# Kernel optimization log

Measured on AMD Instinct MI355X. Metric: run time of the kernel, lower is better.

## Reference

```python
import jax, jax.numpy as jnp
from jax import lax
import numpy as np

N = 87296
NUM_CLASSES = 91
IOU_THRESH = 0.6
MAX_OUT = 100
IMG = 2048.0


def setup_inputs() -> dict:
    key = jax.random.key(0)
    k1, k2, k3, k4, k5 = jax.random.split(key, 5)
    class_logits = jax.random.normal(k1, (N, NUM_CLASSES), dtype=jnp.float32)
    box_regression = jax.random.normal(k2, (N, 4), dtype=jnp.float32)
    box_ctrness = jax.random.normal(k3, (N, 1), dtype=jnp.float32)
    # anchors: valid x1,y1,x2,y2 boxes inside a 2048x2048 image
    ctr = jax.random.uniform(k4, (N, 2), dtype=jnp.float32) * IMG
    wh = jax.random.uniform(k5, (N, 2), dtype=jnp.float32) * 64.0 + 8.0
    anchors = jnp.concatenate([ctr - 0.5 * wh, ctr + 0.5 * wh], axis=1)
    return {"class_logits": class_logits, "box_regression": box_regression,
            "box_ctrness": box_ctrness, "anchors": anchors}


def _decode(rel_codes, anchors):
    # torchvision BoxLinearCoder(normalize_by_size=True).decode
    ctr_x = 0.5 * (anchors[:, 0] + anchors[:, 2])
    ctr_y = 0.5 * (anchors[:, 1] + anchors[:, 3])
    w = anchors[:, 2] - anchors[:, 0]
    h = anchors[:, 3] - anchors[:, 1]
    dl = rel_codes[:, 0] * w
    dt = rel_codes[:, 1] * h
    dr = rel_codes[:, 2] * w
    db = rel_codes[:, 3] * h
    return jnp.stack([ctr_x - dl, ctr_y - dt, ctr_x + dr, ctr_y + db], axis=1)


def _nms_keep(boxes, scores, iou_thresh, max_out):
    # torchvision.ops.nms truncated to max_out; returns indices sorted by score.
    areas = jnp.maximum(boxes[:, 2] - boxes[:, 0], 0.0) * jnp.maximum(boxes[:, 3] - boxes[:, 1], 0.0)

    def body(i, state):
        cur_scores, keep = state
        idx = jnp.argmax(cur_scores)
        keep = keep.at[i].set(idx.astype(jnp.int32))
        b = boxes[idx]
        ix1 = jnp.maximum(b[0], boxes[:, 0])
        iy1 = jnp.maximum(b[1], boxes[:, 1])
        ix2 = jnp.minimum(b[2], boxes[:, 2])
        iy2 = jnp.minimum(b[3], boxes[:, 3])
        inter = jnp.maximum(ix2 - ix1, 0.0) * jnp.maximum(iy2 - iy1, 0.0)
        iou = inter / (areas[idx] + areas - inter)
        # suppress boxes with IoU > thresh (includes the selected box itself)
        cur_scores = jnp.where(iou > iou_thresh, -jnp.inf, cur_scores)
        return cur_scores, keep

    keep0 = jnp.zeros((max_out,), jnp.int32)
    _, keep = lax.fori_loop(0, max_out, body, (scores, keep0))
    return keep


def reference(class_logits, box_regression, box_ctrness, anchors):
    pred_boxes = _decode(box_regression, anchors)              # [N,4]
    cls_scores = jax.nn.sigmoid(class_logits)                  # [N,C]
    ctr_scores = jax.nn.sigmoid(box_ctrness[:, 0])             # [N]
    scores = jnp.sqrt(cls_scores * ctr_scores[:, None])        # [N,C]
    max_scores = jnp.max(scores, axis=1)                       # [N]
    labels = jnp.argmax(scores, axis=1)                        # [N]
    keep = _nms_keep(pred_boxes, max_scores, IOU_THRESH, MAX_OUT)
    return pred_boxes[keep], labels[keep], max_scores[keep]
```

## Files before the change

### kernel.cpp

```cpp
#include <hip/hip_runtime.h>
#include <math.h>

#define N_ANCH 87296
#define NCLS 91
#define NBINS 4096
#define K_CAND 256
#define CAP 512
#define MAX_OUT 100
#define IOU_TH 0.6f
#define T2 1024


__device__ __forceinline__ float sigmoidf_(float x) {
    return 1.0f / (1.0f + expf(-x));
}

__global__ void score_kernel(const float* __restrict__ logits,
                             const float* __restrict__ ctr,
                             float* __restrict__ scores) {
    __shared__ float lds[2 * 64 * 91];
    const int tid  = threadIdx.x;
    const int lane = tid & 63;
    const int w    = tid >> 6;
    const int rowbase = blockIdx.x * 128 + w * 64;

    const float4* g4 = (const float4*)logits + (size_t)rowbase * 91 / 4;
    float4* l4 = (float4*)(lds + w * 5824);
    #pragma unroll
    for (int k = 0; k < 23; ++k) {
        int idx = k * 64 + lane;
        if (idx < 1456) l4[idx] = g4[idx];
    }
    __syncthreads();

    const int i = rowbase + lane;
    const float* row = lds + w * 5824 + lane * 91;
    float m = row[0];
    #pragma unroll
    for (int j = 1; j < NCLS; ++j) m = fmaxf(m, row[j]);
    scores[i] = sqrtf(sigmoidf_(m) * sigmoidf_(ctr[i]));
}

__global__ void __launch_bounds__(T2)
select_nms_kernel(const float* __restrict__ scores,
                  const float* __restrict__ logits,
                  const float* __restrict__ boxreg,
                  const float* __restrict__ anchors,
                  float* __restrict__ out) {
    __shared__ unsigned hist[NBINS];
    __shared__ float    cs[CAP];
    __shared__ int      cidx[CAP];
    __shared__ unsigned cnt;
    __shared__ int      fbin;
    __shared__ float    s_best[16];
    __shared__ int      s_bid[16];
    __shared__ float    s_box[5];
    __shared__ int      s_lab;

    const int tid  = threadIdx.x;
    const int lane = tid & 63;
    const int wid  = tid >> 6;

    for (int b = tid; b < NBINS; b += T2) hist[b] = 0u;
    if (tid == 0) cnt = 0u;
    __syncthreads();

    const float4* s4 = (const float4*)scores;
    #pragma unroll
    for (int k = 0; k < 22; ++k) {
        int idx = k * T2 + tid;
        if (idx < N_ANCH / 4) {
            float4 v = s4[idx];
            int b0 = min(max((int)(v.x * (float)NBINS), 0), NBINS - 1);
            int b1 = min(max((int)(v.y * (float)NBINS), 0), NBINS - 1);
            int b2 = min(max((int)(v.z * (float)NBINS), 0), NBINS - 1);
            int b3 = min(max((int)(v.w * (float)NBINS), 0), NBINS - 1);
            atomicAdd(&hist[b0], 1u);
            atomicAdd(&hist[b1], 1u);
            atomicAdd(&hist[b2], 1u);
            atomicAdd(&hist[b3], 1u);
        }
    }
    __syncthreads();

    if (tid < 64) {
        const uint4* h4 = (const uint4*)hist;
        uint4 c[16];
        #pragma unroll
        for (int q = 0; q < 16; ++q) c[q] = h4[lane * 16 + q];

        unsigned local = 0;
        #pragma unroll
        for (int q = 0; q < 16; ++q) local += c[q].x + c[q].y + c[q].z + c[q].w;

        unsigned p = local;
        #pragma unroll
        for (int d = 1; d < 64; d <<= 1) {
            unsigned t = (unsigned)__shfl_down((int)p, d, 64);
            if (lane + d < 64) p += t;
        }
        unsigned long long mask = __ballot(p >= K_CAND);
        int L = 63 - __clzll(mask);
        unsigned sufAbove = (unsigned)__shfl((int)p, L + 1, 64);
        if (L == 63) sufAbove = 0u;

        if (lane == L) {
            unsigned cum = sufAbove;
            int fb = L * 64;
            bool found = false;
            #pragma unroll
            for (int q = 15; q >= 0; --q) {
                cum += c[q].w; if (!found && cum >= K_CAND) { fb = L * 64 + q * 4 + 3; found = true; }
                cum += c[q].z; if (!found && cum >= K_CAND) { fb = L * 64 + q * 4 + 2; found = true; }
                cum += c[q].y; if (!found && cum >= K_CAND) { fb = L * 64 + q * 4 + 1; found = true; }
                cum += c[q].x; if (!found && cum >= K_CAND) { fb = L * 64 + q * 4 + 0; found = true; }
            }
            fbin = fb;
        }
    }
    __syncthreads();
    const int FB = fbin;

    #pragma unroll
    for (int k = 0; k < 22; ++k) {
        int idx = k * T2 + tid;
        if (idx < N_ANCH / 4) {
            float4 v = s4[idx];
            float vv[4] = {v.x, v.y, v.z, v.w};
            #pragma unroll
            for (int c = 0; c < 4; ++c) {
                float s = vv[c];
                int b = min(max((int)(s * (float)NBINS), 0), NBINS - 1);
                if (b >= FB) {
                    unsigned pos = atomicAdd(&cnt, 1u);
                    if (pos < CAP) { cs[pos] = s; cidx[pos] = idx * 4 + c; }
                }
            }
        }
    }
    __syncthreads();
    const int M = (int)min(cnt, (unsigned)CAP);

    float SC, X1, Y1, X2, Y2, AR;
    int LAB;
    if (tid < M) {
        int i = cidx[tid];
        SC = cs[tid];
        const float* row = logits + (long)i * NCLS;
        float m = row[0];
        int lab = 0;
        #pragma unroll
        for (int j = 1; j < NCLS; ++j) {
            float v = row[j];
            if (v > m) { m = v; lab = j; }
        }
        LAB = lab;
        float a0 = anchors[i * 4 + 0], a1 = anchors[i * 4 + 1];
        float a2 = anchors[i * 4 + 2], a3 = anchors[i * 4 + 3];
        float cx = 0.5f * (a0 + a2);
        float cy = 0.5f * (a1 + a3);
        float w  = a2 - a0;
        float h  = a3 - a1;
        float r0 = boxreg[i * 4 + 0], r1 = boxreg[i * 4 + 1];
        float r2 = boxreg[i * 4 + 2], r3 = boxreg[i * 4 + 3];
        X1 = cx - r0 * w;
        Y1 = cy - r1 * h;
        X2 = cx + r2 * w;
        Y2 = cy + r3 * h;
        AR = fmaxf(X2 - X1, 0.0f) * fmaxf(Y2 - Y1, 0.0f);
    } else {
        SC = -INFINITY;
        X1 = Y1 = X2 = Y2 = AR = 0.0f;
        LAB = 0;
    }
    __syncthreads();

    for (int it = 0; it < MAX_OUT; ++it) {
        float b = SC;
        int id = tid;
        #pragma unroll
        for (int d = 32; d >= 1; d >>= 1) {
            float ob = __shfl_xor(b, d, 64);
            int   oid = __shfl_xor(id, d, 64);
            if (ob > b) { b = ob; id = oid; }
        }
        if (lane == 0) { s_best[wid] = b; s_bid[wid] = id; }
        __syncthreads();
        float gb = s_best[0];
        int gid = s_bid[0];
        #pragma unroll
        for (int w = 1; w < 16; ++w) {
            if (s_best[w] > gb) { gb = s_best[w]; gid = s_bid[w]; }
        }
        if (tid == gid) {
            s_box[0] = X1; s_box[1] = Y1; s_box[2] = X2; s_box[3] = Y2;
            s_box[4] = AR; s_lab = LAB;
        }
        __syncthreads();
        float sx1 = s_box[0], sy1 = s_box[1], sx2 = s_box[2], sy2 = s_box[3];
        float sar = s_box[4];
        int   slab = s_lab;

        if (tid == 0) {
            out[it * 4 + 0] = sx1;
            out[it * 4 + 1] = sy1;
            out[it * 4 + 2] = sx2;
            out[it * 4 + 3] = sy2;
            out[4 * MAX_OUT + it] = (float)slab;
            out[5 * MAX_OUT + it] = gb;
        }

        if (sar == 0.0f) {
            for (int r = it + 1 + tid; r < MAX_OUT; r += T2) {
                out[r * 4 + 0] = sx1;
                out[r * 4 + 1] = sy1;
                out[r * 4 + 2] = sx2;
                out[r * 4 + 3] = sy2;
                out[4 * MAX_OUT + r] = (float)slab;
                out[5 * MAX_OUT + r] = gb;
            }
            return;
        }

        float ix1 = fmaxf(sx1, X1);
        float iy1 = fmaxf(sy1, Y1);
        float ix2 = fminf(sx2, X2);
        float iy2 = fminf(sy2, Y2);
        float inter = fmaxf(ix2 - ix1, 0.0f) * fmaxf(iy2 - iy1, 0.0f);
        float iou = inter / (sar + AR - inter);
        if (iou > IOU_TH) SC = -INFINITY;
        __syncthreads();
    }
}

extern "C" void kernel_launch(void* const* d_in, const int* in_sizes, int n_in,
                              void* d_out, int out_size, void* d_ws, size_t ws_size,
                              hipStream_t stream) {
    const float* logits  = (const float*)d_in[0];
    const float* boxreg  = (const float*)d_in[1];
    const float* ctr     = (const float*)d_in[2];
    const float* anchors = (const float*)d_in[3];
    float* out = (float*)d_out;
    float* scores = (float*)d_ws;

    score_kernel<<<N_ANCH / 128, 128, 0, stream>>>(logits, ctr, scores);
    select_nms_kernel<<<1, T2, 0, stream>>>(scores, logits, boxreg, anchors, out);
}
```

Baseline: 34.20 us.

## Fuse decode, argmax and global histogram into parallel score kernel

The first kernel now also computes each anchor's argmax label, decoded box and area, writing them to workspace, and builds the score histogram with global atomics. This takes the single-block select kernel's full histogram pass over all scores and its scattered per-candidate logits-row reads off the serial path. The cost is extra global writes for every anchor, contended global atomics on the histogram, and an added memset launch.

```diff
diff --git a/kernel.cpp b/kernel.cpp
--- a/kernel.cpp
+++ b/kernel.cpp
@@ -8,6 +8,8 @@
 #define CAP 512
 #define MAX_OUT 100
 #define IOU_TH 0.6f
+#define NB1 682
+#define BT1 128
 #define T2 1024
 
 
@@ -15,17 +17,24 @@
     return 1.0f / (1.0f + expf(-x));
 }
 
-__global__ void score_kernel(const float* __restrict__ logits,
-                             const float* __restrict__ ctr,
-                             float* __restrict__ scores) {
-    __shared__ float lds[2 * 64 * 91];
+__global__ void __launch_bounds__(BT1)
+score_decode_kernel(const float* __restrict__ logits,
+                    const float* __restrict__ boxreg,
+                    const float* __restrict__ ctr,
+                    const float* __restrict__ anchors,
+                    float* __restrict__ scores,
+                    float4* __restrict__ pbox,
+                    float2* __restrict__ pmeta,
+                    unsigned* __restrict__ hist) {
+    __shared__ float pool[2 * 64 * 91];
     const int tid  = threadIdx.x;
     const int lane = tid & 63;
     const int w    = tid >> 6;
-    const int rowbase = blockIdx.x * 128 + w * 64;
-
+    const int bid  = blockIdx.x;
+
+    const int rowbase = bid * BT1 + w * 64;
     const float4* g4 = (const float4*)logits + (size_t)rowbase * 91 / 4;
-    float4* l4 = (float4*)(lds + w * 5824);
+    float4* l4 = (float4*)(pool + w * 5824);
     #pragma unroll
     for (int k = 0; k < 23; ++k) {
         int idx = k * 64 + lane;
@@ -33,25 +42,49 @@
     }
     __syncthreads();
 
-    const int i = rowbase + lane;
-    const float* row = lds + w * 5824 + lane * 91;
+    const int i = bid * BT1 + tid;
+    const float* row = pool + w * 5824 + lane * 91;
     float m = row[0];
+    int lab = 0;
     #pragma unroll
-    for (int j = 1; j < NCLS; ++j) m = fmaxf(m, row[j]);
-    scores[i] = sqrtf(sigmoidf_(m) * sigmoidf_(ctr[i]));
+    for (int j = 1; j < NCLS; ++j) {
+        float v = row[j];
+        if (v > m) { m = v; lab = j; }
+    }
+    const float s = sqrtf(sigmoidf_(m) * sigmoidf_(ctr[i]));
+    scores[i] = s;
+
+    float4 A = ((const float4*)anchors)[i];
+    float4 R = ((const float4*)boxreg)[i];
+    float cx = 0.5f * (A.x + A.z);
+    float cy = 0.5f * (A.y + A.w);
+    float ww = A.z - A.x;
+    float hh = A.w - A.y;
+    float4 bb;
+    bb.x = cx - R.x * ww;
+    bb.y = cy - R.y * hh;
+    bb.z = cx + R.z * ww;
+    bb.w = cy + R.w * hh;
+    pbox[i] = bb;
+    float2 mt;
+    mt.x = fmaxf(bb.z - bb.x, 0.0f) * fmaxf(bb.w - bb.y, 0.0f);
+    mt.y = (float)lab;
+    pmeta[i] = mt;
+
+    const int bin = min(max((int)(s * (float)NBINS), 0), NBINS - 1);
+    atomicAdd(&hist[bin], 1u);
 }
 
 __global__ void __launch_bounds__(T2)
-select_nms_kernel(const float* __restrict__ scores,
-                  const float* __restrict__ logits,
-                  const float* __restrict__ boxreg,
-                  const float* __restrict__ anchors,
+select_nms_kernel(const unsigned* __restrict__ hist,
+                  const float* __restrict__ scores,
+                  const float4* __restrict__ pbox,
+                  const float2* __restrict__ pmeta,
                   float* __restrict__ out) {
-    __shared__ unsigned hist[NBINS];
-    __shared__ float    cs[CAP];
-    __shared__ int      cidx[CAP];
+    __shared__ float    ls[CAP];
+    __shared__ int      lidx[CAP];
     __shared__ unsigned cnt;
-    __shared__ int      fbin;
+    __shared__ int      s_fb;
     __shared__ float    s_best[16];
     __shared__ int      s_bid[16];
     __shared__ float    s_box[5];
@@ -61,27 +94,7 @@
     const int lane = tid & 63;
     const int wid  = tid >> 6;
 
-    for (int b = tid; b < NBINS; b += T2) hist[b] = 0u;
     if (tid == 0) cnt = 0u;
-    __syncthreads();
-
-    const float4* s4 = (const float4*)scores;
-    #pragma unroll
-    for (int k = 0; k < 22; ++k) {
-        int idx = k * T2 + tid;
-        if (idx < N_ANCH / 4) {
-            float4 v = s4[idx];
-            int b0 = min(max((int)(v.x * (float)NBINS), 0), NBINS - 1);
-            int b1 = min(max((int)(v.y * (float)NBINS), 0), NBINS - 1);
-            int b2 = min(max((int)(v.z * (float)NBINS), 0), NBINS - 1);
-            int b3 = min(max((int)(v.w * (float)NBINS), 0), NBINS - 1);
-            atomicAdd(&hist[b0], 1u);
-            atomicAdd(&hist[b1], 1u);
-            atomicAdd(&hist[b2], 1u);
-            atomicAdd(&hist[b3], 1u);
-        }
-    }
-    __syncthreads();
 
     if (tid < 64) {
         const uint4* h4 = (const uint4*)hist;
@@ -115,12 +128,13 @@
                 cum += c[q].y; if (!found && cum >= K_CAND) { fb = L * 64 + q * 4 + 1; found = true; }
                 cum += c[q].x; if (!found && cum >= K_CAND) { fb = L * 64 + q * 4 + 0; found = true; }
             }
-            fbin = fb;
-        }
-    }
-    __syncthreads();
-    const int FB = fbin;
-
+            s_fb = fb;
+        }
+    }
+    __syncthreads();
+    const int FB = s_fb;
+
+    const float4* s4 = (const float4*)scores;
     #pragma unroll
     for (int k = 0; k < 22; ++k) {
         int idx = k * T2 + tid;
@@ -133,7 +147,7 @@
                 int b = min(max((int)(s * (float)NBINS), 0), NBINS - 1);
                 if (b >= FB) {
                     unsigned pos = atomicAdd(&cnt, 1u);
-                    if (pos < CAP) { cs[pos] = s; cidx[pos] = idx * 4 + c; }
+                    if (pos < CAP) { ls[pos] = s; lidx[pos] = idx * 4 + c; }
                 }
             }
         }
@@ -144,30 +158,13 @@
     float SC, X1, Y1, X2, Y2, AR;
     int LAB;
     if (tid < M) {
-        int i = cidx[tid];
-        SC = cs[tid];
-        const float* row = logits + (long)i * NCLS;
-        float m = row[0];
-        int lab = 0;
-        #pragma unroll
-        for (int j = 1; j < NCLS; ++j) {
-            float v = row[j];
-            if (v > m) { m = v; lab = j; }
-        }
-        LAB = lab;
-        float a0 = anchors[i * 4 + 0], a1 = anchors[i * 4 + 1];
-        float a2 = anchors[i * 4 + 2], a3 = anchors[i * 4 + 3];
-        float cx = 0.5f * (a0 + a2);
-        float cy = 0.5f * (a1 + a3);
-        float w  = a2 - a0;
-        float h  = a3 - a1;
-        float r0 = boxreg[i * 4 + 0], r1 = boxreg[i * 4 + 1];
-        float r2 = boxreg[i * 4 + 2], r3 = boxreg[i * 4 + 3];
-        X1 = cx - r0 * w;
-        Y1 = cy - r1 * h;
-        X2 = cx + r2 * w;
-        Y2 = cy + r3 * h;
-        AR = fmaxf(X2 - X1, 0.0f) * fmaxf(Y2 - Y1, 0.0f);
+        int ai = lidx[tid];
+        SC = ls[tid];
+        float4 bb = pbox[ai];
+        float2 mt = pmeta[ai];
+        X1 = bb.x; Y1 = bb.y; X2 = bb.z; Y2 = bb.w;
+        AR = mt.x;
+        LAB = (int)mt.y;
     } else {
         SC = -INFINITY;
         X1 = Y1 = X2 = Y2 = AR = 0.0f;
@@ -241,8 +238,15 @@
     const float* ctr     = (const float*)d_in[2];
     const float* anchors = (const float*)d_in[3];
     float* out = (float*)d_out;
-    float* scores = (float*)d_ws;
-
-    score_kernel<<<N_ANCH / 128, 128, 0, stream>>>(logits, ctr, scores);
-    select_nms_kernel<<<1, T2, 0, stream>>>(scores, logits, boxreg, anchors, out);
-}
+
+    char* ws = (char*)d_ws;
+    unsigned* hist   = (unsigned*)(ws + 0);
+    float*    scores = (float*)(ws + 16384);
+    float4*   pbox   = (float4*)(ws + 365568);
+    float2*   pmeta  = (float2*)(ws + 1762304);
+
+    hipMemsetAsync(ws, 0, 16384, stream);
+    score_decode_kernel<<<NB1, BT1, 0, stream>>>(logits, boxreg, ctr, anchors,
+                                                 scores, pbox, pmeta, hist);
+    select_nms_kernel<<<1, T2, 0, stream>>>(hist, scores, pbox, pmeta, out);
+}
```

Result: slower. 45.81 us (+33.9%).
